# Kernel optimization log

Hardware: AMD Instinct MI355X
Metric: run time of the kernel (lower is better)

## Reference

```python
import jax, jax.numpy as jnp
import numpy as np

N = 100000
E = 1600000
D_IN = 128
D_OUT = 128


def setup_inputs() -> dict:
    key = jax.random.key(0)
    k1, k2, k3, k4, k5, k6 = jax.random.split(key, 6)
    h = jax.random.normal(k1, (N, D_IN), dtype=jnp.float32)
    # deg^{-1/2}-style positive per-node normalization, shape [N,1]
    norm = jax.random.uniform(k2, (N, 1), dtype=jnp.float32, minval=0.05, maxval=1.0)
    weight = jax.random.normal(k3, (D_IN, D_OUT), dtype=jnp.float32) * (1.0 / np.sqrt(D_IN))
    bias = jax.random.normal(k4, (D_OUT,), dtype=jnp.float32) * 0.01
    src = jax.random.randint(k5, (E,), 0, N, dtype=jnp.int32)
    dst = jax.random.randint(k6, (E,), 0, N, dtype=jnp.int32)
    return {"h": h, "norm": norm, "weight": weight, "bias": bias, "src": src, "dst": dst}


def reference(h, norm, weight, bias, src, dst):
    # m = (h @ W) * norm   (per-source-node message)
    m = jnp.matmul(h, weight) * norm            # [N, D_OUT]
    # copy_src + sum: scatter-sum messages from src nodes into dst nodes
    n = jax.ops.segment_sum(m[src], dst, num_segments=h.shape[0])  # [N, D_OUT]
    # destination-side normalization, bias, LeakyReLU(0.2)
    n = n * norm + bias
    return jax.nn.leaky_relu(n, negative_slope=0.2)
```

## Files before the change

### kernel.cpp

```cpp
#include <hip/hip_runtime.h>

#define N_NODES 100000
#define E_EDGES 1600000
#define D 128
#define SHIFT 7
#define BNODES 128
#define NB ((N_NODES + BNODES - 1) / BNODES)

#define CNT_CHUNK 2048
#define CNT_NBLK ((E_EDGES + CNT_CHUNK - 1) / CNT_CHUNK)
#define PREP_NBLK (N_NODES * 32 / 256)
#define SCAT_CHUNK 8192
#define SCAT_PASS 2
#define SCAT_NBLK ((E_EDGES + SCAT_CHUNK - 1) / SCAT_CHUNK)
#define GATH_NBLK (N_NODES / 16)
#define GATH32_NBLK (N_NODES / 8)

#define GROWS 64
#define KCH 32

typedef _Float16       f16x8  __attribute__((ext_vector_type(8)));
typedef float          f32x4  __attribute__((ext_vector_type(4)));
typedef unsigned short u16x8  __attribute__((ext_vector_type(8)));

#define WS_CNT   0
#define WS_POS   784
#define WS_BOFF  1568
#define WS_NOFF  2356
#define WS_EBUF  102400
#define WS_ESRC  (102400 + E_EDGES)
#define WS_HS    (102400 + 2 * E_EDGES)
#define WS_FULL_INTS ((size_t)WS_HS + (size_t)N_NODES * D / 2)
#define WS_MID_INTS  ((size_t)WS_HS)

#define GROW16 256

__global__ __launch_bounds__(256) void prep_count(const float* __restrict__ h,
                                                  const float* __restrict__ norm,
                                                  unsigned short* __restrict__ hs,
                                                  const int* __restrict__ dst,
                                                  int* __restrict__ cnt,
                                                  int prep_blocks) {
    __shared__ int hist[NB];
    const int t = threadIdx.x;
    if ((int)blockIdx.x < prep_blocks) {
        const int idx = blockIdx.x * 256 + t;
        const int node = idx >> 5;
        const int c = (idx & 31) << 2;
        const float nv = norm[node];
        const float4 v = *reinterpret_cast<const float4*>(h + node * D + c);
        float a[4] = {v.x * nv, v.y * nv, v.z * nv, v.w * nv};
        ushort4 o;
        unsigned short* op = reinterpret_cast<unsigned short*>(&o);
        #pragma unroll
        for (int i = 0; i < 4; ++i) {
            unsigned int u = __float_as_uint(a[i]);
            u += 0x7FFFu + ((u >> 16) & 1u);
            op[i] = (unsigned short)(u >> 16);
        }
        *reinterpret_cast<ushort4*>(hs + node * D + c) = o;
        return;
    }
    const int cb = blockIdx.x - prep_blocks;
    const int e0 = cb * CNT_CHUNK;
    const int rem = (E_EDGES - e0 < CNT_CHUNK) ? (E_EDGES - e0) : CNT_CHUNK;
    for (int i = t; i < NB; i += 256) hist[i] = 0;
    __syncthreads();
    if (rem == CNT_CHUNK) {
        const int4* d4 = reinterpret_cast<const int4*>(dst + e0);
        #pragma unroll
        for (int p = 0; p < 2; ++p) {
            const int4 v = d4[p * 256 + t];
            atomicAdd(&hist[v.x >> SHIFT], 1);
            atomicAdd(&hist[v.y >> SHIFT], 1);
            atomicAdd(&hist[v.z >> SHIFT], 1);
            atomicAdd(&hist[v.w >> SHIFT], 1);
        }
    } else {
        for (int i = t; i < rem; i += 256)
            atomicAdd(&hist[dst[e0 + i] >> SHIFT], 1);
    }
    __syncthreads();
    for (int b = t; b < NB; b += 256) {
        const int c = hist[b];
        if (c) atomicAdd(&cnt[b], c);
    }
}

__global__ __launch_bounds__(1024) void scatter_scan(const int* __restrict__ src,
                                                     const int* __restrict__ dst,
                                                     const int* __restrict__ cnt,
                                                     int* __restrict__ pos,
                                                     int* __restrict__ boff,
                                                     int* __restrict__ ebuf) {
    __shared__ int buf[2][1024];
    __shared__ int hist[NB];
    const int t = threadIdx.x;

    const int v = (t < NB) ? cnt[t] : 0;
    int pi = 0;
    buf[0][t] = v;
    __syncthreads();
    #pragma unroll
    for (int o = 1; o < 1024; o <<= 1) {
        const int nv = buf[pi][t] + (t >= o ? buf[pi][t - o] : 0);
        buf[1 - pi][t] = nv;
        pi = 1 - pi;
        __syncthreads();
    }
    const int excl = buf[pi][t] - v;
    if (blockIdx.x == 0) {
        if (t < NB) boff[t] = excl;
        if (t == 0) boff[NB] = E_EDGES;
    }
    if (t < NB) hist[t] = 0;
    __syncthreads();

    const int e0 = blockIdx.x * SCAT_CHUNK;
    const int rem = (E_EDGES - e0 < SCAT_CHUNK) ? (E_EDGES - e0) : SCAT_CHUNK;
    if (rem == SCAT_CHUNK) {
        const int4* d4 = reinterpret_cast<const int4*>(dst + e0);
        #pragma unroll
        for (int p = 0; p < SCAT_PASS; ++p) {
            const int4 vv = d4[p * 1024 + t];
            atomicAdd(&hist[vv.x >> SHIFT], 1);
            atomicAdd(&hist[vv.y >> SHIFT], 1);
            atomicAdd(&hist[vv.z >> SHIFT], 1);
            atomicAdd(&hist[vv.w >> SHIFT], 1);
        }
    } else {
        for (int i = t; i < rem; i += 1024)
            atomicAdd(&hist[dst[e0 + i] >> SHIFT], 1);
    }
    __syncthreads();

    if (t < NB) {
        const int c = hist[t];
        if (c) hist[t] = excl + atomicAdd(&pos[t], c);
    }
    __syncthreads();

    if (rem == SCAT_CHUNK) {
        const int4* d4 = reinterpret_cast<const int4*>(dst + e0);
        const int4* s4 = reinterpret_cast<const int4*>(src + e0);
        #pragma unroll
        for (int p = 0; p < SCAT_PASS; ++p) {
            const int4 dv = d4[p * 1024 + t];
            const int4 sv = s4[p * 1024 + t];
            int pz;
            pz = atomicAdd(&hist[dv.x >> SHIFT], 1);
            ebuf[pz] = (sv.x << SHIFT) | (dv.x & (BNODES - 1));
            pz = atomicAdd(&hist[dv.y >> SHIFT], 1);
            ebuf[pz] = (sv.y << SHIFT) | (dv.y & (BNODES - 1));
            pz = atomicAdd(&hist[dv.z >> SHIFT], 1);
            ebuf[pz] = (sv.z << SHIFT) | (dv.z & (BNODES - 1));
            pz = atomicAdd(&hist[dv.w >> SHIFT], 1);
            ebuf[pz] = (sv.w << SHIFT) | (dv.w & (BNODES - 1));
        }
    } else {
        for (int i = t; i < rem; i += 1024) {
            const int d = dst[e0 + i];
            const int b = d >> SHIFT;
            const int p = atomicAdd(&hist[b], 1);
            ebuf[p] = (src[e0 + i] << SHIFT) | (d & (BNODES - 1));
        }
    }
}

__global__ __launch_bounds__(1024) void coarse_scan(const int* __restrict__ cnt,
                                                    int* __restrict__ boff,
                                                    int* __restrict__ pos) {
    __shared__ int buf[2][1024];
    const int t = threadIdx.x;
    const int v = (t < NB) ? cnt[t] : 0;
    int pi = 0;
    buf[0][t] = v;
    __syncthreads();
    #pragma unroll
    for (int o = 1; o < 1024; o <<= 1) {
        const int nv = buf[pi][t] + (t >= o ? buf[pi][t - o] : 0);
        buf[1 - pi][t] = nv;
        pi = 1 - pi;
        __syncthreads();
    }
    if (t < NB) {
        const int excl = buf[pi][t] - v;
        boff[t] = excl;
        pos[t] = excl;
    }
    if (t == 0) boff[NB] = E_EDGES;
}

__global__ __launch_bounds__(1024) void coarse_scatter(const int* __restrict__ src,
                                                       const int* __restrict__ dst,
                                                       int* __restrict__ pos,
                                                       int* __restrict__ ebuf) {
    __shared__ int hist[NB];
    const int t = threadIdx.x;
    const int e0 = blockIdx.x * SCAT_CHUNK;
    const int rem = (E_EDGES - e0 < SCAT_CHUNK) ? (E_EDGES - e0) : SCAT_CHUNK;
    for (int i = t; i < NB; i += 1024) hist[i] = 0;
    __syncthreads();
    if (rem == SCAT_CHUNK) {
        const int4* d4 = reinterpret_cast<const int4*>(dst + e0);
        #pragma unroll
        for (int p = 0; p < SCAT_PASS; ++p) {
            const int4 v = d4[p * 1024 + t];
            atomicAdd(&hist[v.x >> SHIFT], 1);
            atomicAdd(&hist[v.y >> SHIFT], 1);
            atomicAdd(&hist[v.z >> SHIFT], 1);
            atomicAdd(&hist[v.w >> SHIFT], 1);
        }
    } else {
        for (int i = t; i < rem; i += 1024)
            atomicAdd(&hist[dst[e0 + i] >> SHIFT], 1);
    }
    __syncthreads();
    for (int b = t; b < NB; b += 1024) {
        const int c = hist[b];
        if (c) hist[b] = atomicAdd(&pos[b], c);
    }
    __syncthreads();
    if (rem == SCAT_CHUNK) {
        const int4* d4 = reinterpret_cast<const int4*>(dst + e0);
        const int4* s4 = reinterpret_cast<const int4*>(src + e0);
        #pragma unroll
        for (int p = 0; p < SCAT_PASS; ++p) {
            const int4 dv = d4[p * 1024 + t];
            const int4 sv = s4[p * 1024 + t];
            int pz;
            pz = atomicAdd(&hist[dv.x >> SHIFT], 1);
            ebuf[pz] = (sv.x << SHIFT) | (dv.x & (BNODES - 1));
            pz = atomicAdd(&hist[dv.y >> SHIFT], 1);
            ebuf[pz] = (sv.y << SHIFT) | (dv.y & (BNODES - 1));
            pz = atomicAdd(&hist[dv.z >> SHIFT], 1);
            ebuf[pz] = (sv.z << SHIFT) | (dv.z & (BNODES - 1));
            pz = atomicAdd(&hist[dv.w >> SHIFT], 1);
            ebuf[pz] = (sv.w << SHIFT) | (dv.w & (BNODES - 1));
        }
    } else {
        for (int i = t; i < rem; i += 1024) {
            const int d = dst[e0 + i];
            const int b = d >> SHIFT;
            const int p = atomicAdd(&hist[b], 1);
            ebuf[p] = (src[e0 + i] << SHIFT) | (d & (BNODES - 1));
        }
    }
}

__global__ __launch_bounds__(256) void bin_sort(const int* __restrict__ boff,
                                                const int* __restrict__ ebuf,
                                                int* __restrict__ esrc,
                                                int* __restrict__ noff) {
    __shared__ int hist[BNODES];
    __shared__ int curs[BNODES];
    __shared__ int sbuf[2][BNODES];
    const int t = threadIdx.x;
    const int bin = blockIdx.x;
    if (t < BNODES) hist[t] = 0;
    __syncthreads();
    const int b0 = boff[bin];
    const int b1 = boff[bin + 1];
    for (int i = b0 + t; i < b1; i += 256)
        atomicAdd(&hist[ebuf[i] & (BNODES - 1)], 1);
    __syncthreads();
    if (t < BNODES) sbuf[0][t] = hist[t];
    __syncthreads();
    int pi = 0;
    #pragma unroll
    for (int o = 1; o < BNODES; o <<= 1) {
        if (t < BNODES)
            sbuf[1 - pi][t] = sbuf[pi][t] + (t >= o ? sbuf[pi][t - o] : 0);
        pi = 1 - pi;
        __syncthreads();
    }
    if (t < BNODES) {
        const int base = b0 + sbuf[pi][t] - hist[t];
        curs[t] = base;
        const int node = (bin << SHIFT) + t;
        if (node < N_NODES) noff[node] = base;
    }
    if (bin == 0 && t == 0) noff[N_NODES] = E_EDGES;
    __syncthreads();
    for (int i = b0 + t; i < b1; i += 256) {
        const int w = ebuf[i];
        const int p = atomicAdd(&curs[w & (BNODES - 1)], 1);
        esrc[p] = w >> SHIFT;
    }
}

__device__ __forceinline__ void wprep_body(int tid, const float* __restrict__ Wm,
                                           f16x8* __restrict__ Whs) {
    const int kiter = tid >> 9;
    const int nt = (tid >> 6) & 7;
    const int lane = tid & 63;
    const int q = lane >> 4;
    const int col = nt * 16 + (lane & 15);
    f16x8 v;
    #pragma unroll
    for (int j = 0; j < 8; ++j)
        v[j] = (_Float16)Wm[(kiter * 32 + q * 8 + j) * D + col];
    Whs[tid] = v;
}

__global__ __launch_bounds__(256) void gather_wprep(
    const unsigned short* __restrict__ hs, const int* __restrict__ noff,
    const int* __restrict__ esrc, _Float16* __restrict__ g16,
    const float* __restrict__ Wm, f16x8* __restrict__ Whs)
{
    if ((int)blockIdx.x >= GATH_NBLK) {
        wprep_body((blockIdx.x - GATH_NBLK) * 256 + threadIdx.x, Wm, Whs);
        return;
    }
    const int t = threadIdx.x;
    const int node = blockIdx.x * 16 + (t >> 4);
    const int c = (t & 15) << 3;
    int i = noff[node];
    const int end = noff[node + 1];
    float a[8];
    #pragma unroll
    for (int j = 0; j < 8; ++j) a[j] = 0.f;
    for (; i + 7 < end; i += 8) {
        const int s0 = esrc[i];     const int s1 = esrc[i + 1];
        const int s2 = esrc[i + 2]; const int s3 = esrc[i + 3];
        const int s4 = esrc[i + 4]; const int s5 = esrc[i + 5];
        const int s6 = esrc[i + 6]; const int s7 = esrc[i + 7];
        const u16x8 u0 = *reinterpret_cast<const u16x8*>(hs + s0 * D + c);
        const u16x8 u1 = *reinterpret_cast<const u16x8*>(hs + s1 * D + c);
        const u16x8 u2 = *reinterpret_cast<const u16x8*>(hs + s2 * D + c);
        const u16x8 u3 = *reinterpret_cast<const u16x8*>(hs + s3 * D + c);
        const u16x8 u4 = *reinterpret_cast<const u16x8*>(hs + s4 * D + c);
        const u16x8 u5 = *reinterpret_cast<const u16x8*>(hs + s5 * D + c);
        const u16x8 u6 = *reinterpret_cast<const u16x8*>(hs + s6 * D + c);
        const u16x8 u7 = *reinterpret_cast<const u16x8*>(hs + s7 * D + c);
        #pragma unroll
        for (int j = 0; j < 8; ++j) {
            a[j] += __uint_as_float((unsigned int)u0[j] << 16);
            a[j] += __uint_as_float((unsigned int)u1[j] << 16);
            a[j] += __uint_as_float((unsigned int)u2[j] << 16);
            a[j] += __uint_as_float((unsigned int)u3[j] << 16);
            a[j] += __uint_as_float((unsigned int)u4[j] << 16);
            a[j] += __uint_as_float((unsigned int)u5[j] << 16);
            a[j] += __uint_as_float((unsigned int)u6[j] << 16);
            a[j] += __uint_as_float((unsigned int)u7[j] << 16);
        }
    }
    if (i + 3 < end) {
        const int s0 = esrc[i];     const int s1 = esrc[i + 1];
        const int s2 = esrc[i + 2]; const int s3 = esrc[i + 3];
        const u16x8 u0 = *reinterpret_cast<const u16x8*>(hs + s0 * D + c);
        const u16x8 u1 = *reinterpret_cast<const u16x8*>(hs + s1 * D + c);
        const u16x8 u2 = *reinterpret_cast<const u16x8*>(hs + s2 * D + c);
        const u16x8 u3 = *reinterpret_cast<const u16x8*>(hs + s3 * D + c);
        #pragma unroll
        for (int j = 0; j < 8; ++j) {
            a[j] += __uint_as_float((unsigned int)u0[j] << 16);
            a[j] += __uint_as_float((unsigned int)u1[j] << 16);
            a[j] += __uint_as_float((unsigned int)u2[j] << 16);
            a[j] += __uint_as_float((unsigned int)u3[j] << 16);
        }
        i += 4;
    }
    for (; i < end; ++i) {
        const int s = esrc[i];
        const u16x8 u = *reinterpret_cast<const u16x8*>(hs + s * D + c);
        #pragma unroll
        for (int j = 0; j < 8; ++j)
            a[j] += __uint_as_float((unsigned int)u[j] << 16);
    }
    f16x8 o;
    #pragma unroll
    for (int j = 0; j < 8; ++j) o[j] = (_Float16)a[j];
    *reinterpret_cast<f16x8*>(g16 + node * GROW16 + c) = o;
}

__global__ __launch_bounds__(256) void gemm_mfma_f16g(
    const _Float16* g16, float* out, const f16x8* __restrict__ Whs,
    const float* __restrict__ bias, const float* __restrict__ norm)
{
    __shared__ f16x8 Wlds[2048];
    const int t = threadIdx.x;
    const int row0 = blockIdx.x * 64;

    #pragma unroll
    for (int p = 0; p < 8; ++p)
        reinterpret_cast<float4*>(Wlds)[p * 256 + t] =
            reinterpret_cast<const float4*>(Whs)[p * 256 + t];
    __syncthreads();

    const int lane = t & 63;
    const int strip = t >> 6;
    const int q = lane >> 4;
    const int l15 = lane & 15;

    int mrow = row0 + strip * 16 + l15;
    if (mrow >= N_NODES) mrow = N_NODES - 1;

    f32x4 acc[8];
    #pragma unroll
    for (int i = 0; i < 8; ++i) acc[i] = (f32x4){0.f, 0.f, 0.f, 0.f};

    #pragma unroll
    for (int kiter = 0; kiter < 4; ++kiter) {
        const f16x8 a =
            *reinterpret_cast<const f16x8*>(g16 + mrow * GROW16 + kiter * 32 + q * 8);
        #pragma unroll
        for (int nt = 0; nt < 8; ++nt) {
            const f16x8 b = Wlds[(kiter * 8 + nt) * 64 + lane];
            acc[nt] = __builtin_amdgcn_mfma_f32_16x16x32_f16(a, b, acc[nt], 0, 0, 0);
        }
    }

    __syncthreads();

    float nrm[4];
    int mr[4];
    #pragma unroll
    for (int rgi = 0; rgi < 4; ++rgi) {
        mr[rgi] = row0 + strip * 16 + q * 4 + rgi;
        nrm[rgi] = (mr[rgi] < N_NODES) ? norm[mr[rgi]] : 0.f;
    }
    #pragma unroll
    for (int nt = 0; nt < 8; ++nt) {
        const int col = nt * 16 + l15;
        const float bc = bias[col];
        #pragma unroll
        for (int rgi = 0; rgi < 4; ++rgi) {
            if (mr[rgi] < N_NODES) {
                float v = acc[nt][rgi] * nrm[rgi] + bc;
                v = v > 0.f ? v : 0.2f * v;
                out[mr[rgi] * D + col] = v;
            }
        }
    }
}

__global__ __launch_bounds__(256) void gather_fp32(const float* __restrict__ h,
                                                   const float* __restrict__ norm,
                                                   const int* __restrict__ noff,
                                                   const int* __restrict__ esrc,
                                                   float* __restrict__ g,
                                                   const float* __restrict__ Wm,
                                                   f16x8* __restrict__ Whs) {
    if ((int)blockIdx.x >= GATH32_NBLK) {
        wprep_body((blockIdx.x - GATH32_NBLK) * 256 + threadIdx.x, Wm, Whs);
        return;
    }
    const int t = threadIdx.x;
    const int node = blockIdx.x * 8 + (t >> 5);
    const int c = (t & 31) << 2;
    const int beg = noff[node];
    const int end = noff[node + 1];
    float4 acc = make_float4(0.f, 0.f, 0.f, 0.f);
    for (int i = beg; i < end; ++i) {
        const int s = esrc[i];
        const float nv = norm[s];
        const float4 hv = *reinterpret_cast<const float4*>(h + s * D + c);
        acc.x += hv.x * nv;
        acc.y += hv.y * nv;
        acc.z += hv.z * nv;
        acc.w += hv.w * nv;
    }
    *reinterpret_cast<float4*>(g + node * D + c) = acc;
}

__global__ __launch_bounds__(256) void scatter_kernel(
    const float* __restrict__ h, const float* __restrict__ norm,
    const int* __restrict__ src, const int* __restrict__ dst,
    float* __restrict__ g)
{
    const int idx = blockIdx.x * 256 + threadIdx.x;
    const int e = idx >> 5;
    const int c = (idx & 31) << 2;
    const int s = src[e];
    const int d = dst[e];
    const float nv = norm[s];
    const float4 hv = *reinterpret_cast<const float4*>(h + s * D + c);
    float* gp = g + d * D + c;
    atomicAdd(gp + 0, hv.x * nv);
    atomicAdd(gp + 1, hv.y * nv);
    atomicAdd(gp + 2, hv.z * nv);
    atomicAdd(gp + 3, hv.w * nv);
}

__global__ __launch_bounds__(256) void gemm_mfma(
    float* __restrict__ out, const f16x8* __restrict__ Whs,
    const float* __restrict__ bias, const float* __restrict__ norm)
{
    __shared__ f16x8 Wlds[2048];
    const int t = threadIdx.x;
    const int row0 = blockIdx.x * 64;

    #pragma unroll
    for (int p = 0; p < 8; ++p)
        reinterpret_cast<float4*>(Wlds)[p * 256 + t] =
            reinterpret_cast<const float4*>(Whs)[p * 256 + t];
    __syncthreads();

    const int lane = t & 63;
    const int strip = t >> 6;
    const int q = lane >> 4;
    const int l15 = lane & 15;

    int mrow = row0 + strip * 16 + l15;
    if (mrow >= N_NODES) mrow = N_NODES - 1;

    f32x4 acc[8];
    #pragma unroll
    for (int i = 0; i < 8; ++i) acc[i] = (f32x4){0.f, 0.f, 0.f, 0.f};

    #pragma unroll
    for (int kiter = 0; kiter < 4; ++kiter) {
        const float* gp = out + mrow * D + kiter * 32 + q * 8;
        const float4 ga = *reinterpret_cast<const float4*>(gp);
        const float4 gb = *reinterpret_cast<const float4*>(gp + 4);
        f16x8 a;
        a[0] = (_Float16)ga.x; a[1] = (_Float16)ga.y;
        a[2] = (_Float16)ga.z; a[3] = (_Float16)ga.w;
        a[4] = (_Float16)gb.x; a[5] = (_Float16)gb.y;
        a[6] = (_Float16)gb.z; a[7] = (_Float16)gb.w;
        #pragma unroll
        for (int nt = 0; nt < 8; ++nt) {
            const f16x8 b = Wlds[(kiter * 8 + nt) * 64 + lane];
            acc[nt] = __builtin_amdgcn_mfma_f32_16x16x32_f16(a, b, acc[nt], 0, 0, 0);
        }
    }

    float nrm[4];
    int mr[4];
    #pragma unroll
    for (int rgi = 0; rgi < 4; ++rgi) {
        mr[rgi] = row0 + strip * 16 + q * 4 + rgi;
        nrm[rgi] = (mr[rgi] < N_NODES) ? norm[mr[rgi]] : 0.f;
    }
    #pragma unroll
    for (int nt = 0; nt < 8; ++nt) {
        const int col = nt * 16 + l15;
        const float bc = bias[col];
        #pragma unroll
        for (int rgi = 0; rgi < 4; ++rgi) {
            if (mr[rgi] < N_NODES) {
                float v = acc[nt][rgi] * nrm[rgi] + bc;
                v = v > 0.f ? v : 0.2f * v;
                out[mr[rgi] * D + col] = v;
            }
        }
    }
}

__global__ __launch_bounds__(256) void gemm_epilogue(
    float* __restrict__ out, const float* __restrict__ Wm,
    const float* __restrict__ bias, const float* __restrict__ norm)
{
    __shared__ float gs[GROWS][D + 4];
    __shared__ float Wlds[KCH][D];
    const int t = threadIdx.x;
    const int row0 = blockIdx.x * GROWS;

    #pragma unroll
    for (int p = 0; p < 8; ++p) {
        const int i = p * 256 + t;
        const int r = i >> 5;
        const int c = (i & 31) << 2;
        int gr = row0 + r;
        if (gr >= N_NODES) gr = N_NODES - 1;
        const float4 v = *reinterpret_cast<const float4*>(out + gr * D + c);
        *reinterpret_cast<float4*>(&gs[r][c]) = v;
    }

    const int rg = (t >> 5) * 8;
    const int cb = (t & 31) << 2;

    float4 acc[8];
    #pragma unroll
    for (int i = 0; i < 8; ++i) acc[i] = make_float4(0.f, 0.f, 0.f, 0.f);

    for (int kc = 0; kc < D; kc += KCH) {
        __syncthreads();
        #pragma unroll
        for (int p = 0; p < 4; ++p) {
            const int i = p * 256 + t;
            const int kk = i >> 5;
            const int c = (i & 31) << 2;
            *reinterpret_cast<float4*>(&Wlds[kk][c]) =
                *reinterpret_cast<const float4*>(Wm + (kc + kk) * D + c);
        }
        __syncthreads();

        #pragma unroll
        for (int k4 = 0; k4 < KCH; k4 += 4) {
            float4 wv[4];
            #pragma unroll
            for (int kk = 0; kk < 4; ++kk)
                wv[kk] = *reinterpret_cast<const float4*>(&Wlds[k4 + kk][cb]);
            #pragma unroll
            for (int i = 0; i < 8; ++i) {
                const float4 gv = *reinterpret_cast<const float4*>(&gs[rg + i][kc + k4]);
                acc[i].x += gv.x * wv[0].x; acc[i].y += gv.x * wv[0].y;
                acc[i].z += gv.x * wv[0].z; acc[i].w += gv.x * wv[0].w;
                acc[i].x += gv.y * wv[1].x; acc[i].y += gv.y * wv[1].y;
                acc[i].z += gv.y * wv[1].z; acc[i].w += gv.y * wv[1].w;
                acc[i].x += gv.z * wv[2].x; acc[i].y += gv.z * wv[2].y;
                acc[i].z += gv.z * wv[2].z; acc[i].w += gv.z * wv[2].w;
                acc[i].x += gv.w * wv[3].x; acc[i].y += gv.w * wv[3].y;
                acc[i].z += gv.w * wv[3].z; acc[i].w += gv.w * wv[3].w;
            }
        }
    }

    const float4 b = *reinterpret_cast<const float4*>(bias + cb);
    #pragma unroll
    for (int i = 0; i < 8; ++i) {
        const int gr = row0 + rg + i;
        if (gr < N_NODES) {
            const float nv = norm[gr];
            float4 v;
            v.x = acc[i].x * nv + b.x;
            v.y = acc[i].y * nv + b.y;
            v.z = acc[i].z * nv + b.z;
            v.w = acc[i].w * nv + b.w;
            v.x = v.x > 0.f ? v.x : 0.2f * v.x;
            v.y = v.y > 0.f ? v.y : 0.2f * v.y;
            v.z = v.z > 0.f ? v.z : 0.2f * v.z;
            v.w = v.w > 0.f ? v.w : 0.2f * v.w;
            *reinterpret_cast<float4*>(out + gr * D + cb) = v;
        }
    }
}

extern "C" void kernel_launch(void* const* d_in, const int* in_sizes, int n_in,
                              void* d_out, int out_size, void* d_ws, size_t ws_size,
                              hipStream_t stream) {
    const float* h    = (const float*)d_in[0];
    const float* norm = (const float*)d_in[1];
    const float* Wm   = (const float*)d_in[2];
    const float* bias = (const float*)d_in[3];
    const int*   src  = (const int*)d_in[4];
    const int*   dst  = (const int*)d_in[5];
    float* out = (float*)d_out;
    int* ws = (int*)d_ws;

    if (ws_size >= WS_MID_INTS * 4) {
        int* cnt  = ws + WS_CNT;
        int* pos  = ws + WS_POS;
        int* boff = ws + WS_BOFF;
        int* noff = ws + WS_NOFF;
        int* ebuf = ws + WS_EBUF;
        int* esrc = ws + WS_ESRC;
        unsigned short* hs = (unsigned short*)(ws + WS_HS);
        f16x8* Whs = (f16x8*)ebuf;
        const bool use_bf16 = (ws_size >= WS_FULL_INTS * 4);

        if (use_bf16) {
            hipMemsetAsync(cnt, 0, 2 * 784 * sizeof(int), stream);
            prep_count<<<PREP_NBLK + CNT_NBLK, 256, 0, stream>>>(h, norm, hs, dst, cnt, PREP_NBLK);
            scatter_scan<<<SCAT_NBLK, 1024, 0, stream>>>(src, dst, cnt, pos, boff, ebuf);
            bin_sort<<<NB, 256, 0, stream>>>(boff, ebuf, esrc, noff);
            _Float16* g16 = (_Float16*)out;
            gather_wprep<<<GATH_NBLK + 8, 256, 0, stream>>>(hs, noff, esrc, g16, Wm, Whs);
            gemm_mfma_f16g<<<(N_NODES + 63) / 64, 256, 0, stream>>>(g16, out, Whs, bias, norm);
        } else {
            hipMemsetAsync(cnt, 0, 784 * sizeof(int), stream);
            prep_count<<<CNT_NBLK, 256, 0, stream>>>(h, norm, (unsigned short*)ws, dst, cnt, 0);
            coarse_scan   <<<1, 1024, 0, stream>>>(cnt, boff, pos);
            coarse_scatter<<<SCAT_NBLK, 1024, 0, stream>>>(src, dst, pos, ebuf);
            bin_sort      <<<NB, 256, 0, stream>>>(boff, ebuf, esrc, noff);
            gather_fp32<<<GATH32_NBLK + 8, 256, 0, stream>>>(h, norm, noff, esrc, out, Wm, Whs);
            gemm_mfma<<<(N_NODES + 63) / 64, 256, 0, stream>>>(out, Whs, bias, norm);
        }
    } else {
        hipMemsetAsync(out, 0, (size_t)N_NODES * D * sizeof(float), stream);
        scatter_kernel<<<(E_EDGES * 32) / 256, 256, 0, stream>>>(h, norm, src, dst, out);
        gemm_epilogue<<<(N_NODES + GROWS - 1) / GROWS, 256, 0, stream>>>(out, Wm, bias, norm);
    }
}
```

Before: 236.6 us.

## Fuse per-node bin sort into gather by building per-node source lists in LDS

```diff
diff --git a/kernel.cpp b/kernel.cpp
--- a/kernel.cpp
+++ b/kernel.cpp
@@ -15,6 +15,9 @@
 #define SCAT_NBLK ((E_EDGES + SCAT_CHUNK - 1) / SCAT_CHUNK)
 #define GATH_NBLK (N_NODES / 16)
 #define GATH32_NBLK (N_NODES / 8)
+
+#define CAP_N 96
+#define LSTR 97
 
 #define GROWS 64
 #define KCH 32
@@ -167,6 +170,192 @@
     }
 }
 
+__device__ __forceinline__ void wprep_body(int tid, const float* __restrict__ Wm,
+                                           f16x8* __restrict__ Whs) {
+    const int kiter = tid >> 9;
+    const int nt = (tid >> 6) & 7;
+    const int lane = tid & 63;
+    const int q = lane >> 4;
+    const int col = nt * 16 + (lane & 15);
+    f16x8 v;
+    #pragma unroll
+    for (int j = 0; j < 8; ++j)
+        v[j] = (_Float16)Wm[(kiter * 32 + q * 8 + j) * D + col];
+    Whs[tid] = v;
+}
+
+__global__ __launch_bounds__(256) void gather_direct(
+    const unsigned short* __restrict__ hs, const int* __restrict__ boff,
+    const int* __restrict__ ebuf, _Float16* __restrict__ g16,
+    const float* __restrict__ Wm, f16x8* __restrict__ Whs)
+{
+    if ((int)blockIdx.x >= GATH_NBLK) {
+        wprep_body((blockIdx.x - GATH_NBLK) * 256 + threadIdx.x, Wm, Whs);
+        return;
+    }
+    __shared__ int lists[16][LSTR];
+    __shared__ int lcnt[16];
+    const int t = threadIdx.x;
+    const int g = blockIdx.x;
+    const int bin = g >> 3;
+    const int sub = g & 7;
+    if (t < 16) lcnt[t] = 0;
+    __syncthreads();
+    int b0 = boff[bin];
+    int b1 = boff[bin + 1];
+    b0 = (b0 < 0) ? 0 : ((b0 > E_EDGES) ? E_EDGES : b0);
+    b1 = (b1 < b0) ? b0 : ((b1 > E_EDGES) ? E_EDGES : b1);
+    for (int i = b0 + t; i < b1; i += 256) {
+        const int w = ebuf[i];
+        const int l = w & (BNODES - 1);
+        const unsigned s = (unsigned)w >> SHIFT;
+        if ((l >> 4) == sub && s < (unsigned)N_NODES) {
+            const int p = atomicAdd(&lcnt[l & 15], 1);
+            if (p < CAP_N) lists[l & 15][p] = (int)s;
+        }
+    }
+    __syncthreads();
+
+    const int grp = t >> 4;
+    const int c = (t & 15) << 3;
+    const int node = g * 16 + grp;
+    const int deg = lcnt[grp];
+    float a[8];
+    #pragma unroll
+    for (int j = 0; j < 8; ++j) a[j] = 0.f;
+
+    if (deg <= CAP_N) {
+        const int* lp = lists[grp];
+        int i = 0;
+        for (; i + 7 < deg; i += 8) {
+            const int s0 = lp[i];     const int s1 = lp[i + 1];
+            const int s2 = lp[i + 2]; const int s3 = lp[i + 3];
+            const int s4 = lp[i + 4]; const int s5 = lp[i + 5];
+            const int s6 = lp[i + 6]; const int s7 = lp[i + 7];
+            const u16x8 u0 = *reinterpret_cast<const u16x8*>(hs + s0 * D + c);
+            const u16x8 u1 = *reinterpret_cast<const u16x8*>(hs + s1 * D + c);
+            const u16x8 u2 = *reinterpret_cast<const u16x8*>(hs + s2 * D + c);
+            const u16x8 u3 = *reinterpret_cast<const u16x8*>(hs + s3 * D + c);
+            const u16x8 u4 = *reinterpret_cast<const u16x8*>(hs + s4 * D + c);
+            const u16x8 u5 = *reinterpret_cast<const u16x8*>(hs + s5 * D + c);
+            const u16x8 u6 = *reinterpret_cast<const u16x8*>(hs + s6 * D + c);
+            const u16x8 u7 = *reinterpret_cast<const u16x8*>(hs + s7 * D + c);
+            #pragma unroll
+            for (int j = 0; j < 8; ++j) {
+                a[j] += __uint_as_float((unsigned int)u0[j] << 16);
+                a[j] += __uint_as_float((unsigned int)u1[j] << 16);
+                a[j] += __uint_as_float((unsigned int)u2[j] << 16);
+                a[j] += __uint_as_float((unsigned int)u3[j] << 16);
+                a[j] += __uint_as_float((unsigned int)u4[j] << 16);
+                a[j] += __uint_as_float((unsigned int)u5[j] << 16);
+                a[j] += __uint_as_float((unsigned int)u6[j] << 16);
+                a[j] += __uint_as_float((unsigned int)u7[j] << 16);
+            }
+        }
+        if (i + 3 < deg) {
+            const int s0 = lp[i];     const int s1 = lp[i + 1];
+            const int s2 = lp[i + 2]; const int s3 = lp[i + 3];
+            const u16x8 u0 = *reinterpret_cast<const u16x8*>(hs + s0 * D + c);
+            const u16x8 u1 = *reinterpret_cast<const u16x8*>(hs + s1 * D + c);
+            const u16x8 u2 = *reinterpret_cast<const u16x8*>(hs + s2 * D + c);
+            const u16x8 u3 = *reinterpret_cast<const u16x8*>(hs + s3 * D + c);
+            #pragma unroll
+            for (int j = 0; j < 8; ++j) {
+                a[j] += __uint_as_float((unsigned int)u0[j] << 16);
+                a[j] += __uint_as_float((unsigned int)u1[j] << 16);
+                a[j] += __uint_as_float((unsigned int)u2[j] << 16);
+                a[j] += __uint_as_float((unsigned int)u3[j] << 16);
+            }
+            i += 4;
+        }
+        for (; i < deg; ++i) {
+            const int s = lp[i];
+            const u16x8 u = *reinterpret_cast<const u16x8*>(hs + s * D + c);
+            #pragma unroll
+            for (int j = 0; j < 8; ++j)
+                a[j] += __uint_as_float((unsigned int)u[j] << 16);
+        }
+    } else {
+        const int myl = (sub << 4) | grp;
+        for (int i = b0; i < b1; ++i) {
+            const int w = ebuf[i];
+            const unsigned s = (unsigned)w >> SHIFT;
+            if ((w & (BNODES - 1)) == myl && s < (unsigned)N_NODES) {
+                const u16x8 u = *reinterpret_cast<const u16x8*>(hs + s * D + c);
+                #pragma unroll
+                for (int j = 0; j < 8; ++j)
+                    a[j] += __uint_as_float((unsigned int)u[j] << 16);
+            }
+        }
+    }
+
+    f16x8 o;
+    #pragma unroll
+    for (int j = 0; j < 8; ++j) o[j] = (_Float16)a[j];
+    *reinterpret_cast<f16x8*>(g16 + node * GROW16 + c) = o;
+}
+
+__global__ __launch_bounds__(256) void gemm_mfma_f16g(
+    const _Float16* g16, float* out, const f16x8* __restrict__ Whs,
+    const float* __restrict__ bias, const float* __restrict__ norm)
+{
+    __shared__ f16x8 Wlds[2048];
+    const int t = threadIdx.x;
+    const int row0 = blockIdx.x * 64;
+
+    #pragma unroll
+    for (int p = 0; p < 8; ++p)
+        reinterpret_cast<float4*>(Wlds)[p * 256 + t] =
+            reinterpret_cast<const float4*>(Whs)[p * 256 + t];
+    __syncthreads();
+
+    const int lane = t & 63;
+    const int strip = t >> 6;
+    const int q = lane >> 4;
+    const int l15 = lane & 15;
+
+    int mrow = row0 + strip * 16 + l15;
+    if (mrow >= N_NODES) mrow = N_NODES - 1;
+
+    f32x4 acc[8];
+    #pragma unroll
+    for (int i = 0; i < 8; ++i) acc[i] = (f32x4){0.f, 0.f, 0.f, 0.f};
+
+    #pragma unroll
+    for (int kiter = 0; kiter < 4; ++kiter) {
+        const f16x8 a =
+            *reinterpret_cast<const f16x8*>(g16 + mrow * GROW16 + kiter * 32 + q * 8);
+        #pragma unroll
+        for (int nt = 0; nt < 8; ++nt) {
+            const f16x8 b = Wlds[(kiter * 8 + nt) * 64 + lane];
+            acc[nt] = __builtin_amdgcn_mfma_f32_16x16x32_f16(a, b, acc[nt], 0, 0, 0);
+        }
+    }
+
+    __syncthreads();
+
+    float nrm[4];
+    int mr[4];
+    #pragma unroll
+    for (int rgi = 0; rgi < 4; ++rgi) {
+        mr[rgi] = row0 + strip * 16 + q * 4 + rgi;
+        nrm[rgi] = (mr[rgi] < N_NODES) ? norm[mr[rgi]] : 0.f;
+    }
+    #pragma unroll
+    for (int nt = 0; nt < 8; ++nt) {
+        const int col = nt * 16 + l15;
+        const float bc = bias[col];
+        #pragma unroll
+        for (int rgi = 0; rgi < 4; ++rgi) {
+            if (mr[rgi] < N_NODES) {
+                float v = acc[nt][rgi] * nrm[rgi] + bc;
+                v = v > 0.f ? v : 0.2f * v;
+                out[mr[rgi] * D + col] = v;
+            }
+        }
+    }
+}
+
 __global__ __launch_bounds__(1024) void coarse_scan(const int* __restrict__ cnt,
                                                     int* __restrict__ boff,
                                                     int* __restrict__ pos) {
@@ -286,152 +475,6 @@
         const int w = ebuf[i];
         const int p = atomicAdd(&curs[w & (BNODES - 1)], 1);
         esrc[p] = w >> SHIFT;
-    }
-}
-
-__device__ __forceinline__ void wprep_body(int tid, const float* __restrict__ Wm,
-                                           f16x8* __restrict__ Whs) {
-    const int kiter = tid >> 9;
-    const int nt = (tid >> 6) & 7;
-    const int lane = tid & 63;
-    const int q = lane >> 4;
-    const int col = nt * 16 + (lane & 15);
-    f16x8 v;
-    #pragma unroll
-    for (int j = 0; j < 8; ++j)
-        v[j] = (_Float16)Wm[(kiter * 32 + q * 8 + j) * D + col];
-    Whs[tid] = v;
-}
-
-__global__ __launch_bounds__(256) void gather_wprep(
-    const unsigned short* __restrict__ hs, const int* __restrict__ noff,
-    const int* __restrict__ esrc, _Float16* __restrict__ g16,
-    const float* __restrict__ Wm, f16x8* __restrict__ Whs)
-{
-    if ((int)blockIdx.x >= GATH_NBLK) {
-        wprep_body((blockIdx.x - GATH_NBLK) * 256 + threadIdx.x, Wm, Whs);
-        return;
-    }
-    const int t = threadIdx.x;
-    const int node = blockIdx.x * 16 + (t >> 4);
-    const int c = (t & 15) << 3;
-    int i = noff[node];
-    const int end = noff[node + 1];
-    float a[8];
-    #pragma unroll
-    for (int j = 0; j < 8; ++j) a[j] = 0.f;
-    for (; i + 7 < end; i += 8) {
-        const int s0 = esrc[i];     const int s1 = esrc[i + 1];
-        const int s2 = esrc[i + 2]; const int s3 = esrc[i + 3];
-        const int s4 = esrc[i + 4]; const int s5 = esrc[i + 5];
-        const int s6 = esrc[i + 6]; const int s7 = esrc[i + 7];
-        const u16x8 u0 = *reinterpret_cast<const u16x8*>(hs + s0 * D + c);
-        const u16x8 u1 = *reinterpret_cast<const u16x8*>(hs + s1 * D + c);
-        const u16x8 u2 = *reinterpret_cast<const u16x8*>(hs + s2 * D + c);
-        const u16x8 u3 = *reinterpret_cast<const u16x8*>(hs + s3 * D + c);
-        const u16x8 u4 = *reinterpret_cast<const u16x8*>(hs + s4 * D + c);
-        const u16x8 u5 = *reinterpret_cast<const u16x8*>(hs + s5 * D + c);
-        const u16x8 u6 = *reinterpret_cast<const u16x8*>(hs + s6 * D + c);
-        const u16x8 u7 = *reinterpret_cast<const u16x8*>(hs + s7 * D + c);
-        #pragma unroll
-        for (int j = 0; j < 8; ++j) {
-            a[j] += __uint_as_float((unsigned int)u0[j] << 16);
-            a[j] += __uint_as_float((unsigned int)u1[j] << 16);
-            a[j] += __uint_as_float((unsigned int)u2[j] << 16);
-            a[j] += __uint_as_float((unsigned int)u3[j] << 16);
-            a[j] += __uint_as_float((unsigned int)u4[j] << 16);
-            a[j] += __uint_as_float((unsigned int)u5[j] << 16);
-            a[j] += __uint_as_float((unsigned int)u6[j] << 16);
-            a[j] += __uint_as_float((unsigned int)u7[j] << 16);
-        }
-    }
-    if (i + 3 < end) {
-        const int s0 = esrc[i];     const int s1 = esrc[i + 1];
-        const int s2 = esrc[i + 2]; const int s3 = esrc[i + 3];
-        const u16x8 u0 = *reinterpret_cast<const u16x8*>(hs + s0 * D + c);
-        const u16x8 u1 = *reinterpret_cast<const u16x8*>(hs + s1 * D + c);
-        const u16x8 u2 = *reinterpret_cast<const u16x8*>(hs + s2 * D + c);
-        const u16x8 u3 = *reinterpret_cast<const u16x8*>(hs + s3 * D + c);
-        #pragma unroll
-        for (int j = 0; j < 8; ++j) {
-            a[j] += __uint_as_float((unsigned int)u0[j] << 16);
-            a[j] += __uint_as_float((unsigned int)u1[j] << 16);
-            a[j] += __uint_as_float((unsigned int)u2[j] << 16);
-            a[j] += __uint_as_float((unsigned int)u3[j] << 16);
-        }
-        i += 4;
-    }
-    for (; i < end; ++i) {
-        const int s = esrc[i];
-        const u16x8 u = *reinterpret_cast<const u16x8*>(hs + s * D + c);
-        #pragma unroll
-        for (int j = 0; j < 8; ++j)
-            a[j] += __uint_as_float((unsigned int)u[j] << 16);
-    }
-    f16x8 o;
-    #pragma unroll
-    for (int j = 0; j < 8; ++j) o[j] = (_Float16)a[j];
-    *reinterpret_cast<f16x8*>(g16 + node * GROW16 + c) = o;
-}
-
-__global__ __launch_bounds__(256) void gemm_mfma_f16g(
-    const _Float16* g16, float* out, const f16x8* __restrict__ Whs,
-    const float* __restrict__ bias, const float* __restrict__ norm)
-{
-    __shared__ f16x8 Wlds[2048];
-    const int t = threadIdx.x;
-    const int row0 = blockIdx.x * 64;
-
-    #pragma unroll
-    for (int p = 0; p < 8; ++p)
-        reinterpret_cast<float4*>(Wlds)[p * 256 + t] =
-            reinterpret_cast<const float4*>(Whs)[p * 256 + t];
-    __syncthreads();
-
-    const int lane = t & 63;
-    const int strip = t >> 6;
-    const int q = lane >> 4;
-    const int l15 = lane & 15;
-
-    int mrow = row0 + strip * 16 + l15;
-    if (mrow >= N_NODES) mrow = N_NODES - 1;
-
-    f32x4 acc[8];
-    #pragma unroll
-    for (int i = 0; i < 8; ++i) acc[i] = (f32x4){0.f, 0.f, 0.f, 0.f};
-
-    #pragma unroll
-    for (int kiter = 0; kiter < 4; ++kiter) {
-        const f16x8 a =
-            *reinterpret_cast<const f16x8*>(g16 + mrow * GROW16 + kiter * 32 + q * 8);
-        #pragma unroll
-        for (int nt = 0; nt < 8; ++nt) {
-            const f16x8 b = Wlds[(kiter * 8 + nt) * 64 + lane];
-            acc[nt] = __builtin_amdgcn_mfma_f32_16x16x32_f16(a, b, acc[nt], 0, 0, 0);
-        }
-    }
-
-    __syncthreads();
-
-    float nrm[4];
-    int mr[4];
-    #pragma unroll
-    for (int rgi = 0; rgi < 4; ++rgi) {
-        mr[rgi] = row0 + strip * 16 + q * 4 + rgi;
-        nrm[rgi] = (mr[rgi] < N_NODES) ? norm[mr[rgi]] : 0.f;
-    }
-    #pragma unroll
-    for (int nt = 0; nt < 8; ++nt) {
-        const int col = nt * 16 + l15;
-        const float bc = bias[col];
-        #pragma unroll
-        for (int rgi = 0; rgi < 4; ++rgi) {
-            if (mr[rgi] < N_NODES) {
-                float v = acc[nt][rgi] * nrm[rgi] + bc;
-                v = v > 0.f ? v : 0.2f * v;
-                out[mr[rgi] * D + col] = v;
-            }
-        }
     }
 }
 
@@ -648,18 +691,18 @@
         int* ebuf = ws + WS_EBUF;
         int* esrc = ws + WS_ESRC;
         unsigned short* hs = (unsigned short*)(ws + WS_HS);
-        f16x8* Whs = (f16x8*)ebuf;
         const bool use_bf16 = (ws_size >= WS_FULL_INTS * 4);
 
         if (use_bf16) {
+            f16x8* Whs = (f16x8*)esrc;
             hipMemsetAsync(cnt, 0, 2 * 784 * sizeof(int), stream);
             prep_count<<<PREP_NBLK + CNT_NBLK, 256, 0, stream>>>(h, norm, hs, dst, cnt, PREP_NBLK);
             scatter_scan<<<SCAT_NBLK, 1024, 0, stream>>>(src, dst, cnt, pos, boff, ebuf);
-            bin_sort<<<NB, 256, 0, stream>>>(boff, ebuf, esrc, noff);
             _Float16* g16 = (_Float16*)out;
-            gather_wprep<<<GATH_NBLK + 8, 256, 0, stream>>>(hs, noff, esrc, g16, Wm, Whs);
+            gather_direct<<<GATH_NBLK + 8, 256, 0, stream>>>(hs, boff, ebuf, g16, Wm, Whs);
             gemm_mfma_f16g<<<(N_NODES + 63) / 64, 256, 0, stream>>>(g16, out, Whs, bias, norm);
         } else {
+            f16x8* Whs = (f16x8*)ebuf;
             hipMemsetAsync(cnt, 0, 784 * sizeof(int), stream);
             prep_count<<<CNT_NBLK, 256, 0, stream>>>(h, norm, (unsigned short*)ws, dst, cnt, 0);
             coarse_scan   <<<1, 1024, 0, stream>>>(cnt, boff, pos);
```

Measured after the change: 234.0 us. About the same (-1.1%).
